# Performance work log

Measured on AMD Instinct MI355X. Metric: run time of the kernel, lower is better.

## Reference

```python
import jax, jax.numpy as jnp
import numpy as np

B, T, D, N, L = 8, 2048, 256, 64, 4
LN_EPS = 1e-5


def setup_inputs() -> dict:
    key = jax.random.key(0)
    ks = jax.random.split(key, 8)
    def rn(k, shape, scale=1.0):
        return jax.random.normal(k, shape, dtype=jnp.float32) * scale
    A_init = jnp.log(0.5 + jnp.arange(N, dtype=jnp.float32))  # (N,)
    inp = {
        "sequences": rn(ks[0], (B, T, D)),
        # per-layer stacked params (leading dim L)
        "Wi": rn(ks[1], (L, D, D), 1.0 / np.sqrt(D)),
        "bi": jnp.zeros((L, D), jnp.float32),
        "A_log": jnp.broadcast_to(A_init, (L, D, N)) + 0.0,
        "Cm": rn(ks[2], (L, D, N), 1.0 / np.sqrt(N)),
        "Dp": jnp.ones((L, D), jnp.float32),
        "log_dt": jax.random.uniform(ks[3], (L, D), jnp.float32) * (np.log(0.1) - np.log(0.001)) + np.log(0.001),
        "Wo": rn(ks[4], (L, D, D), 1.0 / np.sqrt(D)),
        "bo": jnp.zeros((L, D), jnp.float32),
        "ln1_g": jnp.ones((L, D), jnp.float32),
        "ln1_b": jnp.zeros((L, D), jnp.float32),
        "ln2_g": jnp.ones((L, D), jnp.float32),
        "ln2_b": jnp.zeros((L, D), jnp.float32),
        "W1": rn(ks[5], (L, D, 4 * D), 1.0 / np.sqrt(D)),
        "b1": jnp.zeros((L, 4 * D), jnp.float32),
        "W2": rn(ks[6], (L, 4 * D, D), 1.0 / np.sqrt(4 * D)),
        "b2": jnp.zeros((L, D), jnp.float32),
        "lnf_g": jnp.ones((D,), jnp.float32),
        "lnf_b": jnp.zeros((D,), jnp.float32),
    }
    return inp


def _ln(x, g, b):
    m = x.mean(-1, keepdims=True)
    v = x.var(-1, keepdims=True)
    return (x - m) / jnp.sqrt(v + LN_EPS) * g + b


def _s4_kernel(A_log_l, Cm_l, log_dt_l, Tlen):
    dt = jnp.exp(log_dt_l)                       # (D,)
    A = -jnp.exp(A_log_l)                        # (D,N)
    A_bar = jnp.exp(A * dt[:, None])             # (D,N)
    B_bar = (A_bar - 1.0) / (A * np.sqrt(N))     # (D,N)
    CB = Cm_l * B_bar                            # (D,N)
    logAb = jnp.log(jnp.clip(A_bar, 1e-10))
    powers = jnp.arange(Tlen, dtype=jnp.float32)
    # (D,N,T) power tensor contracted over N -> (D,T)
    return jnp.einsum('dn,dnt->dt', CB, jnp.exp(logAb[:, :, None] * powers))


def reference(sequences, Wi, bi, A_log, Cm, Dp, log_dt, Wo, bo,
              ln1_g, ln1_b, ln2_g, ln2_b, W1, b1, W2, b2, lnf_g, lnf_b):
    x = sequences  # dropout is identity in eval mode
    Tlen = x.shape[1]
    nfft = 2 * Tlen
    for l in range(L):
        # --- S4D sub-block (pre-norm) ---
        h = _ln(x, ln1_g[l], ln1_b[l])
        u = (h @ Wi[l] + bi[l]).transpose(0, 2, 1)   # (B,D,T)
        K = _s4_kernel(A_log[l], Cm[l], log_dt[l], Tlen)  # (D,T)
        u_f = jnp.fft.rfft(u, n=nfft, axis=-1)
        K_f = jnp.fft.rfft(K, n=nfft, axis=-1)
        y = jnp.fft.irfft(u_f * K_f[None], n=nfft, axis=-1)[..., :Tlen]
        y = y + Dp[l][None, :, None] * u
        y = y.transpose(0, 2, 1) @ Wo[l] + bo[l]
        x = x + y
        # --- MLP sub-block (pre-norm) ---
        h2 = _ln(x, ln2_g[l], ln2_b[l])
        x = x + (jax.nn.gelu(h2 @ W1[l] + b1[l], approximate=False) @ W2[l] + b2[l])
    return _ln(x, lnf_g, lnf_b)
```

## Files before the change

### kernel.cpp

```cpp
#include <hip/hip_runtime.h>
#include <hip/hip_bf16.h>

#define NB 8
#define TT 2048
#define DD 256
#define NN 64
#define LL 4
#define CC 32
#define GG 64
#define BT (NB*TT)

typedef __attribute__((ext_vector_type(8))) short short8;
typedef __attribute__((ext_vector_type(4))) short short4v;
typedef __attribute__((ext_vector_type(4))) float f32x4;

__device__ __forceinline__ float bf2f(__hip_bfloat16 v){ return __bfloat162float(v); }
__device__ __forceinline__ __hip_bfloat16 f2bf(float v){ return __float2bfloat16(v); }
__device__ __forceinline__ short f2bfbits(float v){
  __hip_bfloat16 h = __float2bfloat16(v);
  return __builtin_bit_cast(short, h);
}
__device__ __forceinline__ float bfbits2f(short s){
  __hip_bfloat16 h = __builtin_bit_cast(__hip_bfloat16, s);
  return __bfloat162float(h);
}

__device__ __forceinline__ int get_bf(const void* dtp){
  unsigned u = *(const unsigned*)dtp;
  return ((u >> 16) == (u & 0xFFFFu)) ? 1 : 0;
}

__device__ __forceinline__ float ldin(const void* p, size_t i, int bf){
  return bf ? __bfloat162float(((const __hip_bfloat16*)p)[i]) : ((const float*)p)[i];
}

__device__ __forceinline__ float gelu_f(float x){
  float y = 0.79788456f * fmaf(0.044715f, x*x*x, x);
  float e = __expf(-2.0f * fabsf(y));
  float t = (1.0f - e) / (1.0f + e);
  t = (y >= 0.0f) ? t : -t;
  return 0.5f * x * (1.0f + t);
}

__device__ __forceinline__ void async16(const void* g, void* l){
  __builtin_amdgcn_global_load_lds(
      (const __attribute__((address_space(1))) void*)(unsigned long long)g,
      (__attribute__((address_space(3))) void*)(unsigned long long)l,
      16, 0, 0);
}

__global__ __launch_bounds__(256) void cast_ln_kernel(const void* __restrict__ seq,
    __hip_bfloat16* __restrict__ x, __hip_bfloat16* __restrict__ hN,
    const void* __restrict__ g, const void* __restrict__ b,
    const void* __restrict__ dtp)
{
  int bf = get_bf(dtp);
  int lane = threadIdx.x & 63, w = threadIdx.x >> 6;
  int row = blockIdx.x * 4 + w;
  int c = lane * 4;
  size_t base = (size_t)row*DD + c;
  float v0 = ldin(seq, base+0, bf), v1 = ldin(seq, base+1, bf);
  float v2 = ldin(seq, base+2, bf), v3 = ldin(seq, base+3, bf);
  short4v xk; xk.x=f2bfbits(v0); xk.y=f2bfbits(v1); xk.z=f2bfbits(v2); xk.w=f2bfbits(v3);
  *(short4v*)(x + base) = xk;
  float s = v0+v1+v2+v3;
  #pragma unroll
  for (int o = 1; o < 64; o <<= 1) s += __shfl_xor(s, o);
  float mean = s * (1.0f/DD);
  float d0=v0-mean, d1=v1-mean, d2=v2-mean, d3=v3-mean;
  float sq = d0*d0+d1*d1+d2*d2+d3*d3;
  #pragma unroll
  for (int o = 1; o < 64; o <<= 1) sq += __shfl_xor(sq, o);
  float r = rsqrtf(sq * (1.0f/DD) + 1e-5f);
  short4v hk;
  hk.x = f2bfbits(d0*r*ldin(g,c+0,bf) + ldin(b,c+0,bf));
  hk.y = f2bfbits(d1*r*ldin(g,c+1,bf) + ldin(b,c+1,bf));
  hk.z = f2bfbits(d2*r*ldin(g,c+2,bf) + ldin(b,c+2,bf));
  hk.w = f2bfbits(d3*r*ldin(g,c+3,bf) + ldin(b,c+3,bf));
  *(short4v*)(hN + base) = hk;
}

__global__ __launch_bounds__(256) void transpose_all_kernel(
    const void* __restrict__ Wi, const void* __restrict__ Wo,
    const void* __restrict__ W1, const void* __restrict__ W2,
    __hip_bfloat16* __restrict__ WiT, __hip_bfloat16* __restrict__ WoT,
    __hip_bfloat16* __restrict__ W1T, __hip_bfloat16* __restrict__ W2T,
    const void* __restrict__ dtp)
{
  int bf = get_bf(dtp);
  __shared__ float tile[32][33];
  int id = blockIdx.x;
  const void* W; __hip_bfloat16* Wt; int K, N, l, n0, k0;
  if (id < 256){
    W=Wi; Wt=WiT; K=DD; N=DD;
    int t=id;       l=t>>6; int r=t&63;  n0=(r&7)*32;  k0=(r>>3)*32;
  } else if (id < 512){
    W=Wo; Wt=WoT; K=DD; N=DD;
    int t=id-256;   l=t>>6; int r=t&63;  n0=(r&7)*32;  k0=(r>>3)*32;
  } else if (id < 1536){
    W=W1; Wt=W1T; K=DD; N=4*DD;
    int t=id-512;   l=t>>8; int r=t&255; n0=(r&31)*32; k0=(r>>5)*32;
  } else {
    W=W2; Wt=W2T; K=4*DD; N=DD;
    int t=id-1536;  l=t>>8; int r=t&255; n0=(r&7)*32;  k0=(r>>3)*32;
  }
  size_t zoff = (size_t)l * K * N;
  int tx = threadIdx.x, ty = threadIdx.y;
  #pragma unroll
  for (int i = 0; i < 4; i++)
    tile[ty + i*8][tx] = ldin(W, zoff + (size_t)(k0 + ty + i*8)*N + n0 + tx, bf);
  __syncthreads();
  #pragma unroll
  for (int i = 0; i < 4; i++)
    Wt[zoff + (size_t)(n0 + ty + i*8)*K + k0 + tx] = f2bf(tile[tx][ty + i*8]);
}

__global__ __launch_bounds__(256) void gemm_w1_kernel(
    const __hip_bfloat16* __restrict__ A, const __hip_bfloat16* __restrict__ Wt,
    const void* __restrict__ bias, size_t boff,
    __hip_bfloat16* __restrict__ C, int N, int K, const void* __restrict__ dtp)
{
  int bf = get_bf(dtp);
  __shared__ __align__(16) char smem[24576];
  short (*Als)[128][32] = (short(*)[128][32])smem;
  short (*Bls)[64][32]  = (short(*)[64][32])(smem + 16384);
  short* Cls = (short*)smem;
  int tid = threadIdx.x;
  int lane = tid & 63, w = tid >> 6;
  int quad = lane >> 4, row16 = lane & 15;
  int wm = (w >> 1) * 64, wn = (w & 1) * 32;
  int bm = blockIdx.x * 128, bn = blockIdx.y * 64;
  const short* Ag = (const short*)A + (size_t)bm * K;
  const short* Bg = (const short*)Wt + (size_t)bn * K;
  int r0 = tid >> 2, c8 = (tid & 3) * 8;
  f32x4 acc[4][2] = {};
  for (int k0 = 0; k0 < K; k0 += 64){
    #pragma unroll
    for (int kc = 0; kc < 2; kc++){
      async16(Ag + (size_t)r0*K      + k0 + kc*32 + c8, &Als[kc][r0][c8]);
      async16(Ag + (size_t)(64+r0)*K + k0 + kc*32 + c8, &Als[kc][64+r0][c8]);
      async16(Bg + (size_t)r0*K      + k0 + kc*32 + c8, &Bls[kc][r0][c8]);
    }
    __syncthreads();
    #pragma unroll
    for (int kc = 0; kc < 2; kc++){
      short8 af[4], bfr[2];
      #pragma unroll
      for (int i = 0; i < 4; i++)
        af[i] = *(const short8*)&Als[kc][wm + i*16 + row16][quad*8];
      #pragma unroll
      for (int j = 0; j < 2; j++)
        bfr[j] = *(const short8*)&Bls[kc][wn + j*16 + row16][quad*8];
      #pragma unroll
      for (int i = 0; i < 4; i++)
        #pragma unroll
        for (int j = 0; j < 2; j++)
          acc[i][j] = __builtin_amdgcn_mfma_f32_16x16x32_bf16(af[i], bfr[j], acc[i][j], 0, 0, 0);
    }
    __syncthreads();
  }
  #pragma unroll
  for (int i = 0; i < 4; i++){
    #pragma unroll
    for (int j = 0; j < 2; j++){
      int col = wn + j*16 + row16;
      float bv = ldin(bias, boff + bn + col, bf);
      #pragma unroll
      for (int r = 0; r < 4; r++){
        int row = wm + i*16 + quad*4 + r;
        Cls[row*72 + col] = f2bfbits(gelu_f(acc[i][j][r] + bv));
      }
    }
  }
  __syncthreads();
  #pragma unroll
  for (int p = 0; p < 4; p++){
    int ch = p*256 + tid;
    int row = ch >> 3, c0 = (ch & 7) * 8;
    short8 v = *(const short8*)&Cls[row*72 + c0];
    *(short8*)&C[(size_t)(bm + row)*N + bn + c0] = v;
  }
}

__global__ __launch_bounds__(256) void gemm_wi_lf_kernel(
    const __hip_bfloat16* __restrict__ A, const __hip_bfloat16* __restrict__ Wt,
    const void* __restrict__ bias, size_t boff,
    __hip_bfloat16* __restrict__ uout, __hip_bfloat16* __restrict__ LFS,
    const float* __restrict__ abT, int K, const void* __restrict__ dtp)
{
  int bf = get_bf(dtp);
  __shared__ __align__(16) char smem[73728];
  short (*Als)[32][32]  = (short(*)[32][32])smem;
  short (*Bls)[256][32] = (short(*)[256][32])(smem + 8192);
  float* Cls = (float*)smem;
  int tid = threadIdx.x, lane = tid & 63, w = tid >> 6;
  int quad = lane >> 4, row16 = lane & 15;
  int wn = w * 64;
  int bm = blockIdx.x * 32;
  const short* Ag = (const short*)A + (size_t)bm * K;
  const short* Bg = (const short*)Wt;
  f32x4 acc[2][4] = {};
  for (int k0 = 0; k0 < K; k0 += 128){
    #pragma unroll
    for (int p = 0; p < 2; p++){
      int ch = p*256 + tid;
      int kc = ch >> 7, r = (ch >> 2) & 31, c = (ch & 3) * 8;
      async16(Ag + (size_t)r*K + k0 + kc*32 + c, &Als[kc][r][c]);
    }
    #pragma unroll
    for (int p = 0; p < 16; p++){
      int ch = p*256 + tid;
      int kc = ch >> 10, r = (ch >> 2) & 255, c = (ch & 3) * 8;
      async16(Bg + (size_t)r*K + k0 + kc*32 + c, &Bls[kc][r][c]);
    }
    __syncthreads();
    #pragma unroll
    for (int kc = 0; kc < 4; kc++){
      short8 af[2], bfr[4];
      #pragma unroll
      for (int i = 0; i < 2; i++)
        af[i] = *(const short8*)&Als[kc][i*16 + row16][quad*8];
      #pragma unroll
      for (int j = 0; j < 4; j++)
        bfr[j] = *(const short8*)&Bls[kc][wn + j*16 + row16][quad*8];
      #pragma unroll
      for (int i = 0; i < 2; i++)
        #pragma unroll
        for (int j = 0; j < 4; j++)
          acc[i][j] = __builtin_amdgcn_mfma_f32_16x16x32_bf16(af[i], bfr[j], acc[i][j], 0, 0, 0);
    }
    __syncthreads();
  }
  #pragma unroll
  for (int i = 0; i < 2; i++)
    #pragma unroll
    for (int j = 0; j < 4; j++){
      int col = wn + j*16 + row16;
      #pragma unroll
      for (int r = 0; r < 4; r++){
        int row = i*16 + quad*4 + r;
        Cls[row*260 + col] = acc[i][j][r];
      }
    }
  __syncthreads();
  {
    int row = tid >> 3, l7 = tid & 7;
    size_t rbase = (size_t)(bm + row)*DD;
    #pragma unroll
    for (int q = 0; q < 8; q++){
      int c0 = l7*4 + q*32;
      float4 t = *(const float4*)&Cls[row*260 + c0];
      float v0 = t.x + ldin(bias, boff+c0+0, bf);
      float v1 = t.y + ldin(bias, boff+c0+1, bf);
      float v2 = t.z + ldin(bias, boff+c0+2, bf);
      float v3 = t.w + ldin(bias, boff+c0+3, bf);
      float4 wbk; wbk.x=v0; wbk.y=v1; wbk.z=v2; wbk.w=v3;
      *(float4*)&Cls[row*260 + c0] = wbk;
      short4v pk; pk.x=f2bfbits(v0); pk.y=f2bfbits(v1); pk.z=f2bfbits(v2); pk.w=f2bfbits(v3);
      *(short4v*)&uout[rbase + c0] = pk;
    }
  }
  __syncthreads();
  {
    int d = tid;
    int cix = bm >> 5;
    float ab[NN], accn[NN];
    #pragma unroll
    for (int n = 0; n < NN; n++){ ab[n] = abT[n*DD + d]; accn[n] = 0.0f; }
    #pragma unroll 1
    for (int s = 0; s < CC; s++){
      float uv = Cls[s*260 + d];
      #pragma unroll
      for (int n = 0; n < NN; n++) accn[n] = fmaf(ab[n], accn[n], uv);
    }
    #pragma unroll
    for (int n = 0; n < NN; n++)
      LFS[((size_t)cix*NN + n)*DD + d] = f2bf(accn[n]);
  }
}

__global__ __launch_bounds__(256) void s4_scan_kernel(__hip_bfloat16* __restrict__ LFS,
    const float* __restrict__ AbarCT)
{
  int d = threadIdx.x;
  int n = blockIdx.x & (NN-1), b = blockIdx.x >> 6;
  float a = AbarCT[n*DD + d];
  float s = 0.0f;
  #pragma unroll 1
  for (int g = 0; g < GG; g++){
    size_t idx = ((size_t)((b*GG + g)*NN) + n)*DD + d;
    float lf = bf2f(LFS[idx]);
    LFS[idx] = f2bf(s);
    s = fmaf(a, s, lf);
  }
}

__global__ __launch_bounds__(256) void gemm_wo_recur_kernel(
    const __hip_bfloat16* __restrict__ uB, const __hip_bfloat16* __restrict__ Sin,
    const float* __restrict__ abT, const float* __restrict__ cbT,
    const void* __restrict__ Dp, size_t dpoff,
    const __hip_bfloat16* __restrict__ Wt, const void* __restrict__ bias, size_t boff,
    const __hip_bfloat16* __restrict__ resx, __hip_bfloat16* __restrict__ xout,
    const void* __restrict__ g, size_t goff, const void* __restrict__ bb, size_t bboff,
    __hip_bfloat16* __restrict__ hout, int K)
{
  int bf = get_bf(Dp);
  __shared__ __align__(16) char smem[81920];
  short* Afull = (short*)smem;
  short (*Bls)[256][32] = (short(*)[256][32])(smem + 16384);
  float* Cls = (float*)(smem + 16384);
  int tid = threadIdx.x, lane = tid & 63, w = tid >> 6;
  int quad = lane >> 4, row16 = lane & 15;
  int wn = w * 64;
  int bm = blockIdx.x * 32;
  {
    int d = tid;
    float st[NN], ab[NN], cb[NN];
    const __hip_bfloat16* sbase = Sin + ((size_t)(bm >> 5) * NN)*DD + d;
    #pragma unroll
    for (int n = 0; n < NN; n++){
      st[n] = bf2f(sbase[(size_t)n*DD]);
      ab[n] = abT[n*DD + d];
      cb[n] = cbT[n*DD + d];
    }
    float dp = ldin(Dp, dpoff + d, bf);
    const __hip_bfloat16* up = uB + (size_t)bm*DD + d;
    short* ya = Afull + (d >> 5)*1024 + (d & 31);
    float uv = bf2f(up[0]);
    #pragma unroll 1
    for (int tau = 0; tau < CC; tau++){
      float uvn = (tau < CC-1) ? bf2f(up[(size_t)(tau+1)*DD]) : 0.0f;
      float a0 = 0.0f, a1 = 0.0f, a2 = 0.0f, a3 = 0.0f;
      #pragma unroll
      for (int n = 0; n < NN; n += 4){
        st[n+0] = fmaf(ab[n+0], st[n+0], uv); a0 = fmaf(cb[n+0], st[n+0], a0);
        st[n+1] = fmaf(ab[n+1], st[n+1], uv); a1 = fmaf(cb[n+1], st[n+1], a1);
        st[n+2] = fmaf(ab[n+2], st[n+2], uv); a2 = fmaf(cb[n+2], st[n+2], a2);
        st[n+3] = fmaf(ab[n+3], st[n+3], uv); a3 = fmaf(cb[n+3], st[n+3], a3);
      }
      ya[tau*32] = f2bfbits(fmaf(dp, uv, (a0 + a1) + (a2 + a3)));
      uv = uvn;
    }
  }
  __syncthreads();
  const short* Bg = (const short*)Wt;
  f32x4 acc[2][4] = {};
  for (int k0 = 0; k0 < K; k0 += 128){
    #pragma unroll
    for (int p = 0; p < 16; p++){
      int ch = p*256 + tid;
      int kc = ch >> 10, r = (ch >> 2) & 255, c = (ch & 3) * 8;
      async16(Bg + (size_t)r*K + k0 + kc*32 + c, &Bls[kc][r][c]);
    }
    __syncthreads();
    #pragma unroll
    for (int kc = 0; kc < 4; kc++){
      short8 af[2], bfr[4];
      #pragma unroll
      for (int i = 0; i < 2; i++)
        af[i] = *(const short8*)&Afull[((k0 >> 5) + kc)*1024 + (i*16 + row16)*32 + quad*8];
      #pragma unroll
      for (int j = 0; j < 4; j++)
        bfr[j] = *(const short8*)&Bls[kc][wn + j*16 + row16][quad*8];
      #pragma unroll
      for (int i = 0; i < 2; i++)
        #pragma unroll
        for (int j = 0; j < 4; j++)
          acc[i][j] = __builtin_amdgcn_mfma_f32_16x16x32_bf16(af[i], bfr[j], acc[i][j], 0, 0, 0);
    }
    __syncthreads();
  }
  #pragma unroll
  for (int i = 0; i < 2; i++)
    #pragma unroll
    for (int j = 0; j < 4; j++){
      int col = wn + j*16 + row16;
      #pragma unroll
      for (int r = 0; r < 4; r++){
        int row = i*16 + quad*4 + r;
        Cls[row*260 + col] = acc[i][j][r];
      }
    }
  __syncthreads();
  int row = tid >> 3, l7 = tid & 7;
  size_t rbase = (size_t)(bm + row)*DD;
  float v[8][4];
  #pragma unroll
  for (int q = 0; q < 8; q++){
    int c0 = l7*4 + q*32;
    float4 t = *(const float4*)&Cls[row*260 + c0];
    short4v rx = *(const short4v*)&resx[rbase + c0];
    v[q][0] = t.x + ldin(bias, boff+c0+0, bf) + bfbits2f(rx.x);
    v[q][1] = t.y + ldin(bias, boff+c0+1, bf) + bfbits2f(rx.y);
    v[q][2] = t.z + ldin(bias, boff+c0+2, bf) + bfbits2f(rx.z);
    v[q][3] = t.w + ldin(bias, boff+c0+3, bf) + bfbits2f(rx.w);
    short4v pk; pk.x=f2bfbits(v[q][0]); pk.y=f2bfbits(v[q][1]);
    pk.z=f2bfbits(v[q][2]); pk.w=f2bfbits(v[q][3]);
    *(short4v*)&xout[rbase + c0] = pk;
  }
  float s = 0.0f, sq = 0.0f;
  #pragma unroll
  for (int q = 0; q < 8; q++)
    #pragma unroll
    for (int e = 0; e < 4; e++){ s += v[q][e]; sq += v[q][e]*v[q][e]; }
  #pragma unroll
  for (int o = 1; o < 8; o <<= 1){ s += __shfl_xor(s, o); sq += __shfl_xor(sq, o); }
  float mean = s * (1.0f/DD);
  float rstd = rsqrtf(sq * (1.0f/DD) - mean*mean + 1e-5f);
  #pragma unroll
  for (int q = 0; q < 8; q++){
    int c0 = l7*4 + q*32;
    short4v pk;
    pk.x = f2bfbits((v[q][0]-mean)*rstd*ldin(g,goff+c0+0,bf) + ldin(bb,bboff+c0+0,bf));
    pk.y = f2bfbits((v[q][1]-mean)*rstd*ldin(g,goff+c0+1,bf) + ldin(bb,bboff+c0+1,bf));
    pk.z = f2bfbits((v[q][2]-mean)*rstd*ldin(g,goff+c0+2,bf) + ldin(bb,bboff+c0+2,bf));
    pk.w = f2bfbits((v[q][3]-mean)*rstd*ldin(g,goff+c0+3,bf) + ldin(bb,bboff+c0+3,bf));
    *(short4v*)&hout[rbase + c0] = pk;
  }
}

template <int MODE>
__global__ __launch_bounds__(256) void gemm_row_kernel(
    const __hip_bfloat16* __restrict__ A, const __hip_bfloat16* __restrict__ Wt,
    const void* __restrict__ bias, size_t boff,
    const __hip_bfloat16* __restrict__ resx, __hip_bfloat16* __restrict__ xout,
    const void* __restrict__ g, size_t goff,
    const void* __restrict__ bb, size_t bboff,
    __hip_bfloat16* __restrict__ hout, void* __restrict__ vout,
    int K, const void* __restrict__ dtp)
{
  int bf = get_bf(dtp);
  __shared__ __align__(16) char smem[73728];
  short (*Als)[32][32]  = (short(*)[32][32])smem;
  short (*Bls)[256][32] = (short(*)[256][32])(smem + 8192);
  float* Cls = (float*)smem;
  int tid = threadIdx.x, lane = tid & 63, w = tid >> 6;
  int quad = lane >> 4, row16 = lane & 15;
  int wn = w * 64;
  int bm = blockIdx.x * 32;
  const short* Ag = (const short*)A + (size_t)bm * K;
  const short* Bg = (const short*)Wt;
  f32x4 acc[2][4] = {};
  for (int k0 = 0; k0 < K; k0 += 128){
    #pragma unroll
    for (int p = 0; p < 2; p++){
      int ch = p*256 + tid;
      int kc = ch >> 7, r = (ch >> 2) & 31, c = (ch & 3) * 8;
      async16(Ag + (size_t)r*K + k0 + kc*32 + c, &Als[kc][r][c]);
    }
    #pragma unroll
    for (int p = 0; p < 16; p++){
      int ch = p*256 + tid;
      int kc = ch >> 10, r = (ch >> 2) & 255, c = (ch & 3) * 8;
      async16(Bg + (size_t)r*K + k0 + kc*32 + c, &Bls[kc][r][c]);
    }
    __syncthreads();
    #pragma unroll
    for (int kc = 0; kc < 4; kc++){
      short8 af[2], bfr[4];
      #pragma unroll
      for (int i = 0; i < 2; i++)
        af[i] = *(const short8*)&Als[kc][i*16 + row16][quad*8];
      #pragma unroll
      for (int j = 0; j < 4; j++)
        bfr[j] = *(const short8*)&Bls[kc][wn + j*16 + row16][quad*8];
      #pragma unroll
      for (int i = 0; i < 2; i++)
        #pragma unroll
        for (int j = 0; j < 4; j++)
          acc[i][j] = __builtin_amdgcn_mfma_f32_16x16x32_bf16(af[i], bfr[j], acc[i][j], 0, 0, 0);
    }
    __syncthreads();
  }
  #pragma unroll
  for (int i = 0; i < 2; i++)
    #pragma unroll
    for (int j = 0; j < 4; j++){
      int col = wn + j*16 + row16;
      #pragma unroll
      for (int r = 0; r < 4; r++){
        int row = i*16 + quad*4 + r;
        Cls[row*260 + col] = acc[i][j][r];
      }
    }
  __syncthreads();
  int row = tid >> 3, l7 = tid & 7;
  size_t rbase = (size_t)(bm + row)*DD;
  float v[8][4];
  #pragma unroll
  for (int q = 0; q < 8; q++){
    int c0 = l7*4 + q*32;
    float4 t = *(const float4*)&Cls[row*260 + c0];
    short4v rx = *(const short4v*)&resx[rbase + c0];
    v[q][0] = t.x + ldin(bias, boff+c0+0, bf) + bfbits2f(rx.x);
    v[q][1] = t.y + ldin(bias, boff+c0+1, bf) + bfbits2f(rx.y);
    v[q][2] = t.z + ldin(bias, boff+c0+2, bf) + bfbits2f(rx.z);
    v[q][3] = t.w + ldin(bias, boff+c0+3, bf) + bfbits2f(rx.w);
    if (MODE == 1){
      short4v pk; pk.x=f2bfbits(v[q][0]); pk.y=f2bfbits(v[q][1]);
      pk.z=f2bfbits(v[q][2]); pk.w=f2bfbits(v[q][3]);
      *(short4v*)&xout[rbase + c0] = pk;
    }
  }
  float s = 0.0f, sq = 0.0f;
  #pragma unroll
  for (int q = 0; q < 8; q++)
    #pragma unroll
    for (int e = 0; e < 4; e++){ s += v[q][e]; sq += v[q][e]*v[q][e]; }
  #pragma unroll
  for (int o = 1; o < 8; o <<= 1){ s += __shfl_xor(s, o); sq += __shfl_xor(sq, o); }
  float mean = s * (1.0f/DD);
  float rstd = rsqrtf(sq * (1.0f/DD) - mean*mean + 1e-5f);
  #pragma unroll
  for (int q = 0; q < 8; q++){
    int c0 = l7*4 + q*32;
    float o0 = (v[q][0]-mean)*rstd*ldin(g,goff+c0+0,bf) + ldin(bb,bboff+c0+0,bf);
    float o1 = (v[q][1]-mean)*rstd*ldin(g,goff+c0+1,bf) + ldin(bb,bboff+c0+1,bf);
    float o2 = (v[q][2]-mean)*rstd*ldin(g,goff+c0+2,bf) + ldin(bb,bboff+c0+2,bf);
    float o3 = (v[q][3]-mean)*rstd*ldin(g,goff+c0+3,bf) + ldin(bb,bboff+c0+3,bf);
    if (MODE == 1){
      short4v pk; pk.x=f2bfbits(o0); pk.y=f2bfbits(o1); pk.z=f2bfbits(o2); pk.w=f2bfbits(o3);
      *(short4v*)&hout[rbase + c0] = pk;
    } else {
      if (bf){
        short4v pk; pk.x=f2bfbits(o0); pk.y=f2bfbits(o1); pk.z=f2bfbits(o2); pk.w=f2bfbits(o3);
        *(short4v*)&((__hip_bfloat16*)vout)[rbase + c0] = pk;
      } else {
        float4 pk; pk.x=o0; pk.y=o1; pk.z=o2; pk.w=o3;
        *(float4*)&((float*)vout)[rbase + c0] = pk;
      }
    }
  }
}

__global__ __launch_bounds__(256) void s4_setup_kernel(const void* __restrict__ A_log,
    const void* __restrict__ Cm, const void* __restrict__ log_dt,
    float* __restrict__ AbarT, float* __restrict__ AbarCT, float* __restrict__ cbT,
    const void* __restrict__ dtp)
{
  int bf = get_bf(dtp);
  int d = threadIdx.x, n = blockIdx.x, l = blockIdx.y;
  float dtv = expf(ldin(log_dt, (size_t)l*DD + d, bf));
  float A   = -expf(ldin(A_log, ((size_t)l*DD + d)*NN + n, bf));
  float ab  = expf(A * dtv);
  float bbv = (fabsf(A) > 1e-8f) ? (ab - 1.0f) / (A * 8.0f) : dtv * 0.125f;
  float cb  = ldin(Cm, ((size_t)l*DD + d)*NN + n, bf) * bbv;
  size_t o = ((size_t)l*NN + n)*DD + d;
  AbarT[o] = ab;
  cbT[o]   = cb;
  float p = ab;
  #pragma unroll
  for (int i = 0; i < 5; i++) p *= p;
  AbarCT[o] = p;
}

extern "C" void kernel_launch(void* const* d_in, const int* in_sizes, int n_in,
                              void* d_out, int out_size, void* d_ws, size_t ws_size,
                              hipStream_t stream) {
  const void* seq   = d_in[0];
  const void* Wi    = d_in[1];
  const void* bi    = d_in[2];
  const void* A_log = d_in[3];
  const void* Cm    = d_in[4];
  const void* Dp    = d_in[5];
  const void* logdt = d_in[6];
  const void* Wo    = d_in[7];
  const void* bo    = d_in[8];
  const void* ln1g  = d_in[9];
  const void* ln1b  = d_in[10];
  const void* ln2g  = d_in[11];
  const void* ln2b  = d_in[12];
  const void* W1    = d_in[13];
  const void* b1    = d_in[14];
  const void* W2    = d_in[15];
  const void* b2    = d_in[16];
  const void* lnfg  = d_in[17];
  const void* lnfb  = d_in[18];

  char* ws = (char*)d_ws;
  size_t off = 0;
  __hip_bfloat16* x   = (__hip_bfloat16*)(ws + off); off += (size_t)BT*DD*2;
  __hip_bfloat16* uB  = (__hip_bfloat16*)(ws + off); off += (size_t)BT*DD*2;
  __hip_bfloat16* hN  = (__hip_bfloat16*)(ws + off); off += (size_t)BT*DD*2;
  __hip_bfloat16* mid = (__hip_bfloat16*)(ws + off); off += (size_t)BT*4*DD*2;
  __hip_bfloat16* LFS = (__hip_bfloat16*)(ws + off); off += (size_t)NB*GG*NN*DD*2;
  __hip_bfloat16* WiT = (__hip_bfloat16*)(ws + off); off += (size_t)LL*DD*DD*2;
  __hip_bfloat16* WoT = (__hip_bfloat16*)(ws + off); off += (size_t)LL*DD*DD*2;
  __hip_bfloat16* W1T = (__hip_bfloat16*)(ws + off); off += (size_t)LL*DD*4*DD*2;
  __hip_bfloat16* W2T = (__hip_bfloat16*)(ws + off); off += (size_t)LL*4*DD*DD*2;
  float* AbarT  = (float*)(ws + off); off += (size_t)LL*NN*DD*4;
  float* AbarCT = (float*)(ws + off); off += (size_t)LL*NN*DD*4;
  float* cbT    = (float*)(ws + off); off += (size_t)LL*NN*DD*4;

  (void)in_sizes; (void)n_in; (void)out_size; (void)ws_size;

  cast_ln_kernel<<<BT/4, 256, 0, stream>>>(seq, x, hN, ln1g, ln1b, Dp);
  transpose_all_kernel<<<2560, dim3(32,8), 0, stream>>>(
      Wi, Wo, W1, W2, WiT, WoT, W1T, W2T, Dp);
  s4_setup_kernel<<<dim3(NN, LL), DD, 0, stream>>>(A_log, Cm, logdt, AbarT, AbarCT, cbT, Dp);

  for (int l = 0; l < LL; l++){
    const size_t oD  = (size_t)l*DD;
    const size_t o4D = (size_t)l*4*DD;
    const float* abT  = AbarT  + (size_t)l*NN*DD;
    const float* abCT = AbarCT + (size_t)l*NN*DD;
    const float* cbTl = cbT    + (size_t)l*NN*DD;

    gemm_wi_lf_kernel<<<BT/32, 256, 0, stream>>>(
        hN, WiT + (size_t)l*DD*DD, bi, oD, uB, LFS, abT, DD, Dp);
    s4_scan_kernel<<<NB*NN, 256, 0, stream>>>(LFS, abCT);
    gemm_wo_recur_kernel<<<BT/32, 256, 0, stream>>>(
        uB, LFS, abT, cbTl, Dp, oD,
        WoT + (size_t)l*DD*DD, bo, oD, x, x,
        ln2g, oD, ln2b, oD, hN, DD);

    gemm_w1_kernel<<<dim3(BT/128, 4*DD/64), 256, 0, stream>>>(
        hN, W1T + (size_t)l*DD*4*DD, b1, o4D, mid, 4*DD, DD, Dp);
    if (l < LL-1){
      gemm_row_kernel<1><<<BT/32, 256, 0, stream>>>(
          mid, W2T + (size_t)l*4*DD*DD, b2, oD, x, x,
          ln1g, (size_t)(l+1)*DD, ln1b, (size_t)(l+1)*DD, hN, nullptr, 4*DD, Dp);
    } else {
      gemm_row_kernel<2><<<BT/32, 256, 0, stream>>>(
          mid, W2T + (size_t)l*4*DD*DD, b2, oD, x, nullptr,
          lnfg, 0, lnfb, 0, nullptr, d_out, 4*DD, Dp);
    }
  }
}
```

Before: 649.6 us.

## Split recurrence state across thread pairs and widen Wo GEMM block to 512 threads

The chunk-recurrence part of the fused Wo GEMM now uses two threads per channel, each owning 32 of the 64 state modes, and combines their partial sums with a lane shuffle. The u tile is staged into LDS asynchronously instead of being read from global memory each step. The GEMM and LayerNorm epilogue are re-tiled for 8 waves with a smaller K step, and LDS shrinks to 64KB. The scan kernel's loop is also unrolled by four so loads are issued ahead of the dependent FMAs. The aim is to cut per-thread register pressure and serial latency in the recurrence. The cost is an extra shuffle per step, half the threads idle on the store, and more barriers in the GEMM loop.

```diff
diff --git a/kernel.cpp b/kernel.cpp
--- a/kernel.cpp
+++ b/kernel.cpp
@@ -285,17 +285,27 @@
   int d = threadIdx.x;
   int n = blockIdx.x & (NN-1), b = blockIdx.x >> 6;
   float a = AbarCT[n*DD + d];
+  size_t base = ((size_t)(b*GG)*NN + n)*DD + d;
+  const size_t gs = (size_t)NN*DD;
   float s = 0.0f;
   #pragma unroll 1
-  for (int g = 0; g < GG; g++){
-    size_t idx = ((size_t)((b*GG + g)*NN) + n)*DD + d;
-    float lf = bf2f(LFS[idx]);
-    LFS[idx] = f2bf(s);
-    s = fmaf(a, s, lf);
-  }
-}
-
-__global__ __launch_bounds__(256) void gemm_wo_recur_kernel(
+  for (int g = 0; g < GG; g += 4){
+    size_t i0 = base + (size_t)(g+0)*gs;
+    size_t i1 = base + (size_t)(g+1)*gs;
+    size_t i2 = base + (size_t)(g+2)*gs;
+    size_t i3 = base + (size_t)(g+3)*gs;
+    float lf0 = bf2f(LFS[i0]);
+    float lf1 = bf2f(LFS[i1]);
+    float lf2 = bf2f(LFS[i2]);
+    float lf3 = bf2f(LFS[i3]);
+    LFS[i0] = f2bf(s); s = fmaf(a, s, lf0);
+    LFS[i1] = f2bf(s); s = fmaf(a, s, lf1);
+    LFS[i2] = f2bf(s); s = fmaf(a, s, lf2);
+    LFS[i3] = f2bf(s); s = fmaf(a, s, lf3);
+  }
+}
+
+__global__ __launch_bounds__(512, 4) void gemm_wo_recur_kernel(
     const __hip_bfloat16* __restrict__ uB, const __hip_bfloat16* __restrict__ Sin,
     const float* __restrict__ abT, const float* __restrict__ cbT,
     const void* __restrict__ Dp, size_t dpoff,
@@ -305,67 +315,77 @@
     __hip_bfloat16* __restrict__ hout, int K)
 {
   int bf = get_bf(Dp);
-  __shared__ __align__(16) char smem[81920];
-  short* Afull = (short*)smem;
-  short (*Bls)[256][32] = (short(*)[256][32])(smem + 16384);
-  float* Cls = (float*)(smem + 16384);
+  __shared__ __align__(16) char smem[65536];
+  short* Uls   = (short*)smem;
+  short* Afull = (short*)(smem + 16384);
+  short (*Bls)[256][32] = (short(*)[256][32])(smem + 32768);
+  float* Cls = (float*)smem;
   int tid = threadIdx.x, lane = tid & 63, w = tid >> 6;
   int quad = lane >> 4, row16 = lane & 15;
-  int wn = w * 64;
   int bm = blockIdx.x * 32;
   {
-    int d = tid;
-    float st[NN], ab[NN], cb[NN];
-    const __hip_bfloat16* sbase = Sin + ((size_t)(bm >> 5) * NN)*DD + d;
-    #pragma unroll
-    for (int n = 0; n < NN; n++){
-      st[n] = bf2f(sbase[(size_t)n*DD]);
-      ab[n] = abT[n*DD + d];
-      cb[n] = cbT[n*DD + d];
-    }
-    float dp = ldin(Dp, dpoff + d, bf);
-    const __hip_bfloat16* up = uB + (size_t)bm*DD + d;
+    const short* ug = (const short*)uB + (size_t)bm * DD;
+    async16(ug + tid*8,        Uls + tid*8);
+    async16(ug + 4096 + tid*8, Uls + 4096 + tid*8);
+  }
+  int d = tid >> 1, ng = tid & 1, nb = ng * 32;
+  float st[32], ab[32], cb[32];
+  {
+    const __hip_bfloat16* sbase = Sin + ((size_t)(bm >> 5) * NN + nb)*DD + d;
+    const float* abase = abT + (size_t)nb*DD + d;
+    const float* cbase = cbT + (size_t)nb*DD + d;
+    #pragma unroll
+    for (int i = 0; i < 32; i++){
+      st[i] = bf2f(sbase[(size_t)i*DD]);
+      ab[i] = abase[(size_t)i*DD];
+      cb[i] = cbase[(size_t)i*DD];
+    }
+  }
+  float dp = ldin(Dp, dpoff + d, bf);
+  __syncthreads();
+  {
     short* ya = Afull + (d >> 5)*1024 + (d & 31);
-    float uv = bf2f(up[0]);
     #pragma unroll 1
     for (int tau = 0; tau < CC; tau++){
-      float uvn = (tau < CC-1) ? bf2f(up[(size_t)(tau+1)*DD]) : 0.0f;
+      float uv = bfbits2f(Uls[tau*DD + d]);
       float a0 = 0.0f, a1 = 0.0f, a2 = 0.0f, a3 = 0.0f;
       #pragma unroll
-      for (int n = 0; n < NN; n += 4){
-        st[n+0] = fmaf(ab[n+0], st[n+0], uv); a0 = fmaf(cb[n+0], st[n+0], a0);
-        st[n+1] = fmaf(ab[n+1], st[n+1], uv); a1 = fmaf(cb[n+1], st[n+1], a1);
-        st[n+2] = fmaf(ab[n+2], st[n+2], uv); a2 = fmaf(cb[n+2], st[n+2], a2);
-        st[n+3] = fmaf(ab[n+3], st[n+3], uv); a3 = fmaf(cb[n+3], st[n+3], a3);
+      for (int i = 0; i < 32; i += 4){
+        st[i+0] = fmaf(ab[i+0], st[i+0], uv); a0 = fmaf(cb[i+0], st[i+0], a0);
+        st[i+1] = fmaf(ab[i+1], st[i+1], uv); a1 = fmaf(cb[i+1], st[i+1], a1);
+        st[i+2] = fmaf(ab[i+2], st[i+2], uv); a2 = fmaf(cb[i+2], st[i+2], a2);
+        st[i+3] = fmaf(ab[i+3], st[i+3], uv); a3 = fmaf(cb[i+3], st[i+3], a3);
       }
-      ya[tau*32] = f2bfbits(fmaf(dp, uv, (a0 + a1) + (a2 + a3)));
-      uv = uvn;
+      float tot = (a0 + a1) + (a2 + a3);
+      tot += __shfl_xor(tot, 1);
+      if (ng == 0) ya[tau*32] = f2bfbits(fmaf(dp, uv, tot));
     }
   }
   __syncthreads();
   const short* Bg = (const short*)Wt;
-  f32x4 acc[2][4] = {};
-  for (int k0 = 0; k0 < K; k0 += 128){
-    #pragma unroll
-    for (int p = 0; p < 16; p++){
-      int ch = p*256 + tid;
-      int kc = ch >> 10, r = (ch >> 2) & 255, c = (ch & 3) * 8;
+  int wn = w * 32;
+  f32x4 acc[2][2] = {};
+  for (int k0 = 0; k0 < K; k0 += 64){
+    #pragma unroll
+    for (int p = 0; p < 4; p++){
+      int ch = p*512 + tid;
+      int kc = ch >> 10, rem = ch & 1023, r = rem >> 2, c = (rem & 3) * 8;
       async16(Bg + (size_t)r*K + k0 + kc*32 + c, &Bls[kc][r][c]);
     }
     __syncthreads();
     #pragma unroll
-    for (int kc = 0; kc < 4; kc++){
-      short8 af[2], bfr[4];
+    for (int kc = 0; kc < 2; kc++){
+      short8 af[2], bfr[2];
       #pragma unroll
       for (int i = 0; i < 2; i++)
         af[i] = *(const short8*)&Afull[((k0 >> 5) + kc)*1024 + (i*16 + row16)*32 + quad*8];
       #pragma unroll
-      for (int j = 0; j < 4; j++)
+      for (int j = 0; j < 2; j++)
         bfr[j] = *(const short8*)&Bls[kc][wn + j*16 + row16][quad*8];
       #pragma unroll
       for (int i = 0; i < 2; i++)
         #pragma unroll
-        for (int j = 0; j < 4; j++)
+        for (int j = 0; j < 2; j++)
           acc[i][j] = __builtin_amdgcn_mfma_f32_16x16x32_bf16(af[i], bfr[j], acc[i][j], 0, 0, 0);
     }
     __syncthreads();
@@ -373,7 +393,7 @@
   #pragma unroll
   for (int i = 0; i < 2; i++)
     #pragma unroll
-    for (int j = 0; j < 4; j++){
+    for (int j = 0; j < 2; j++){
       int col = wn + j*16 + row16;
       #pragma unroll
       for (int r = 0; r < 4; r++){
@@ -382,12 +402,12 @@
       }
     }
   __syncthreads();
-  int row = tid >> 3, l7 = tid & 7;
+  int row = tid >> 4, l4 = tid & 15;
   size_t rbase = (size_t)(bm + row)*DD;
-  float v[8][4];
-  #pragma unroll
-  for (int q = 0; q < 8; q++){
-    int c0 = l7*4 + q*32;
+  float v[4][4];
+  #pragma unroll
+  for (int q = 0; q < 4; q++){
+    int c0 = l4*4 + q*64;
     float4 t = *(const float4*)&Cls[row*260 + c0];
     short4v rx = *(const short4v*)&resx[rbase + c0];
     v[q][0] = t.x + ldin(bias, boff+c0+0, bf) + bfbits2f(rx.x);
@@ -400,16 +420,16 @@
   }
   float s = 0.0f, sq = 0.0f;
   #pragma unroll
-  for (int q = 0; q < 8; q++)
+  for (int q = 0; q < 4; q++)
     #pragma unroll
     for (int e = 0; e < 4; e++){ s += v[q][e]; sq += v[q][e]*v[q][e]; }
   #pragma unroll
-  for (int o = 1; o < 8; o <<= 1){ s += __shfl_xor(s, o); sq += __shfl_xor(sq, o); }
+  for (int o = 1; o < 16; o <<= 1){ s += __shfl_xor(s, o); sq += __shfl_xor(sq, o); }
   float mean = s * (1.0f/DD);
   float rstd = rsqrtf(sq * (1.0f/DD) - mean*mean + 1e-5f);
   #pragma unroll
-  for (int q = 0; q < 8; q++){
-    int c0 = l7*4 + q*32;
+  for (int q = 0; q < 4; q++){
+    int c0 = l4*4 + q*64;
     short4v pk;
     pk.x = f2bfbits((v[q][0]-mean)*rstd*ldin(g,goff+c0+0,bf) + ldin(bb,bboff+c0+0,bf));
     pk.y = f2bfbits((v[q][1]-mean)*rstd*ldin(g,goff+c0+1,bf) + ldin(bb,bboff+c0+1,bf));
@@ -609,7 +629,7 @@
     gemm_wi_lf_kernel<<<BT/32, 256, 0, stream>>>(
         hN, WiT + (size_t)l*DD*DD, bi, oD, uB, LFS, abT, DD, Dp);
     s4_scan_kernel<<<NB*NN, 256, 0, stream>>>(LFS, abCT);
-    gemm_wo_recur_kernel<<<BT/32, 256, 0, stream>>>(
+    gemm_wo_recur_kernel<<<BT/32, 512, 0, stream>>>(
         uB, LFS, abT, cbTl, Dp, oD,
         WoT + (size_t)l*DD*DD, bo, oD, x, x,
         ln2g, oD, ln2b, oD, hN, DD);
```

Result: faster. 616.7 us (-5.1%).
